# Performance work log

Hardware: AMD Instinct MI355X
Metric: run time of the kernel (lower is better)

## Reference

```python
import jax, jax.numpy as jnp
import numpy as np

EPS = 1e-3  # BN1d eps from norm_cfg


def _vfe_layer(x, W, gamma, beta, max_out, cat_max):
    """x: (N, M, Cin); W: (Cout, Cin) torch Linear layout; BN in training mode
    (batch stats over voxels N and points M per channel), then ReLU."""
    y = jnp.einsum('nmc,oc->nmo', x, W)            # (N, M, Cout)
    mean = y.mean(axis=(0, 1))                     # (Cout,)
    var = y.var(axis=(0, 1))                       # biased var, as BN uses
    y = (y - mean) * jax.lax.rsqrt(var + EPS) * gamma + beta
    pointwise = jax.nn.relu(y)                     # (N, M, Cout)
    if not max_out:
        return pointwise
    aggregated = pointwise.max(axis=1, keepdims=True)  # (N, 1, Cout)
    if not cat_max:
        return aggregated[:, 0, :]                 # (N, Cout)
    M = x.shape[1]
    repeated = jnp.broadcast_to(aggregated, (x.shape[0], M, aggregated.shape[2]))
    return jnp.concatenate([pointwise, repeated], axis=2)  # (N, M, 2*Cout)


def setup_inputs() -> dict:
    key = jax.random.key(0)
    ks = jax.random.split(key, 3)
    N, M, C = 20000, 64, 10
    return {
        'voxel_feats': jax.random.normal(ks[0], (N, M, C), dtype=jnp.float32),
        'W0': jax.random.normal(ks[1], (64, C), dtype=jnp.float32) * (1.0 / np.sqrt(C)),
        'gamma0': jnp.ones((64,), dtype=jnp.float32),
        'beta0': jnp.zeros((64,), dtype=jnp.float32),
        'W1': jax.random.normal(ks[2], (128, 128), dtype=jnp.float32) * (1.0 / np.sqrt(128)),
        'gamma1': jnp.ones((128,), dtype=jnp.float32),
        'beta1': jnp.zeros((128,), dtype=jnp.float32),
    }


def reference(voxel_feats, W0, gamma0, beta0, W1, gamma1, beta1):
    # layer 0: in=10 -> out=64, max_out=True, cat_max=True -> (N, M, 128)
    x = _vfe_layer(voxel_feats, W0, gamma0, beta0, max_out=True, cat_max=True)
    # layer 1 (last): in=128 -> out=128, max_out=True, cat_max=False -> (N, 128)
    x = _vfe_layer(x, W1, gamma1, beta1, max_out=True, cat_max=False)
    return x
```

## Files before the change

### kernel.cpp

```cpp
#include <hip/hip_runtime.h>

#define NVOX 20000
#define MPTS 64
#define CIN  10
#define NM   (NVOX*MPTS)
#define EPSBN 1e-3f

#define WS_SCALE0 0
#define WS_SHIFT0 64
#define WS_SCALE1 128
#define WS_SHIFT1 256

#define NB0   512
#define P0STR 72
#define NB1   1024
#define NBF   1536

typedef short bf16x8 __attribute__((ext_vector_type(8)));
typedef float f32x4  __attribute__((ext_vector_type(4)));

__device__ __forceinline__ unsigned short f2bf(float f) {
    union { float f; unsigned u; } v; v.f = f;
    unsigned r = v.u + 0x7FFFu + ((v.u >> 16) & 1u);
    return (unsigned short)(r >> 16);
}

__global__ __launch_bounds__(256) void k_stats0(const float* __restrict__ x,
                                                float* __restrict__ p0) {
    __shared__ float sm[4][P0STR];
    float sx[CIN];
    float sxx[55];
#pragma unroll
    for (int i = 0; i < CIN; i++) sx[i] = 0.f;
#pragma unroll
    for (int k = 0; k < 55; k++) sxx[k] = 0.f;

    const int t = threadIdx.x;
    const int tid = blockIdx.x * 256 + t;

    for (int g = tid; g < NM / 2; g += NB0 * 256) {
        const float4* xp = (const float4*)(x + (size_t)g * 20);
        float4 a = xp[0], b = xp[1], c = xp[2], d = xp[3], e = xp[4];
        float v0[CIN] = {a.x, a.y, a.z, a.w, b.x, b.y, b.z, b.w, c.x, c.y};
        float v1[CIN] = {c.z, c.w, d.x, d.y, d.z, d.w, e.x, e.y, e.z, e.w};
#pragma unroll
        for (int i = 0; i < CIN; i++) sx[i] += v0[i] + v1[i];
#pragma unroll
        for (int i = 0; i < CIN; i++)
#pragma unroll
            for (int j = 0; j <= i; j++)
                sxx[i * (i + 1) / 2 + j] += v0[i] * v0[j] + v1[i] * v1[j];
    }

    const int l = t & 63, w = t >> 6;
#pragma unroll
    for (int i = 0; i < CIN; i++) {
        float v = sx[i];
#pragma unroll
        for (int off = 32; off; off >>= 1) v += __shfl_xor(v, off, 64);
        if (l == 0) sm[w][i] = v;
    }
#pragma unroll
    for (int k = 0; k < 55; k++) {
        float v = sxx[k];
#pragma unroll
        for (int off = 32; off; off >>= 1) v += __shfl_xor(v, off, 64);
        if (l == 0) sm[w][10 + k] = v;
    }
    __syncthreads();
    if (t < 65)
        p0[blockIdx.x * P0STR + t] = sm[0][t] + sm[1][t] + sm[2][t] + sm[3][t];
}

__global__ void k_finalize0(const float* __restrict__ p0, float* __restrict__ ws,
                            const float* __restrict__ w0,
                            const float* __restrict__ gamma0, const float* __restrict__ beta0) {
    __shared__ float s[P0STR];
    const int t = threadIdx.x;
    if (t < 65) {
        float acc = 0.f;
#pragma unroll 8
        for (int r = 0; r < NB0; r++) acc += p0[r * P0STR + t];
        s[t] = acc;
    }
    __syncthreads();
    if (t < 64) {
        float w[CIN];
#pragma unroll
        for (int i = 0; i < CIN; i++) w[i] = w0[t * CIN + i];
        float m = 0.f;
#pragma unroll
        for (int i = 0; i < CIN; i++) m += w[i] * s[i];
        m *= (1.f / NM);
        float q = 0.f;
#pragma unroll
        for (int i = 0; i < CIN; i++)
#pragma unroll
            for (int j = 0; j <= i; j++)
                q += ((i == j) ? 1.f : 2.f) * w[i] * w[j] * s[10 + i * (i + 1) / 2 + j];
        q *= (1.f / NM);
        float var = q - m * m;
        float scale = gamma0[t] * rsqrtf(var + EPSBN);
        ws[WS_SCALE0 + t] = scale;
        ws[WS_SHIFT0 + t] = beta0[t] - m * scale;
    }
}

__global__ void k_finalize1(const float* __restrict__ p1, float* __restrict__ ws,
                            const float* __restrict__ gamma1, const float* __restrict__ beta1) {
    __shared__ float sm[2][4];
    const int c = blockIdx.x;
    const int t = threadIdx.x, l = t & 63, w = t >> 6;
    float s = 0.f, qq = 0.f;
#pragma unroll
    for (int r = t; r < NB1; r += 256) {
        s  += p1[(size_t)r * 256 + c];
        qq += p1[(size_t)r * 256 + 128 + c];
    }
#pragma unroll
    for (int off = 32; off; off >>= 1) { s += __shfl_xor(s, off, 64); qq += __shfl_xor(qq, off, 64); }
    if (l == 0) { sm[0][w] = s; sm[1][w] = qq; }
    __syncthreads();
    if (t == 0) {
        float S = sm[0][0] + sm[0][1] + sm[0][2] + sm[0][3];
        float Q = sm[1][0] + sm[1][1] + sm[1][2] + sm[1][3];
        float m = S * (1.f / NM);
        float var = Q * (1.f / NM) - m * m;
        float scale = gamma1[c] * rsqrtf(var + EPSBN);
        ws[WS_SCALE1 + c] = scale;
        ws[WS_SHIFT1 + c] = beta1[c] - m * scale;
    }
}

template <bool STATS>
__global__ __launch_bounds__(256) void k_pass(const float* __restrict__ x,
                                              const float* __restrict__ w0,
                                              const float* __restrict__ w1,
                                              const float* __restrict__ ws,
                                              float* __restrict__ pout) {
    __shared__ float xs[MPTS * CIN];
    __shared__ unsigned short zB[MPTS * 72];
    __shared__ unsigned short aggB[64];
    __shared__ float red[4 * 64];
    __shared__ float pbuf[256];

    const int t  = threadIdx.x;
    const int l  = t & 63;
    const int w  = t >> 6;
    const int lr = l & 15;
    const int lg = l >> 4;

    const int ch = t & 63;
    const int q  = t >> 6;
    float w0r[CIN];
#pragma unroll
    for (int i = 0; i < CIN; i++) w0r[i] = w0[ch * CIN + i];
    const float sc0 = ws[WS_SCALE0 + ch];
    const float sh0 = ws[WS_SHIFT0 + ch];

    bf16x8 wfrag[2][4];
#pragma unroll
    for (int njl = 0; njl < 2; njl++) {
        const float* wrow = w1 + (32 * w + 16 * njl + lr) * 128;
#pragma unroll
        for (int ks = 0; ks < 4; ks++) {
            float4 a = *(const float4*)(wrow + 32 * ks + 8 * lg);
            float4 b = *(const float4*)(wrow + 32 * ks + 8 * lg + 4);
            bf16x8 f;
            f[0] = (short)f2bf(a.x); f[1] = (short)f2bf(a.y);
            f[2] = (short)f2bf(a.z); f[3] = (short)f2bf(a.w);
            f[4] = (short)f2bf(b.x); f[5] = (short)f2bf(b.y);
            f[6] = (short)f2bf(b.z); f[7] = (short)f2bf(b.w);
            wfrag[njl][ks] = f;
        }
    }

    float sc1[2], sh1[2];
    if (!STATS) {
#pragma unroll
        for (int njl = 0; njl < 2; njl++) {
            int col = 32 * w + 16 * njl + lr;
            sc1[njl] = ws[WS_SCALE1 + col];
            sh1[njl] = ws[WS_SHIFT1 + col];
        }
    }
    float as_[2] = {0.f, 0.f}, aq[2] = {0.f, 0.f};

    const int nblk = STATS ? NB1 : NBF;
    for (int n = blockIdx.x; n < NVOX; n += nblk) {
        const float* xv = x + (size_t)n * (MPTS * CIN);
        if (t < 160) ((float4*)xs)[t] = ((const float4*)xv)[t];
        __syncthreads();

        float pm = 0.f;
#pragma unroll
        for (int k = 0; k < 16; k++) {
            int p = q * 16 + k;
            const float* xp = xs + p * CIN;
            float y = xp[0] * w0r[0] + xp[1] * w0r[1] + xp[2] * w0r[2] + xp[3] * w0r[3] +
                      xp[4] * w0r[4] + xp[5] * w0r[5] + xp[6] * w0r[6] + xp[7] * w0r[7] +
                      xp[8] * w0r[8] + xp[9] * w0r[9];
            float v = fmaxf(fmaf(y, sc0, sh0), 0.f);
            zB[p * 72 + ch] = f2bf(v);
            pm = fmaxf(pm, v);
        }
        red[q * 64 + ch] = pm;
        __syncthreads();
        if (t < 64) {
            float m = fmaxf(fmaxf(red[t], red[64 + t]), fmaxf(red[128 + t], red[192 + t]));
            aggB[t] = f2bf(m);
        }
        __syncthreads();

        bf16x8 afrag[4][2];
#pragma unroll
        for (int mi = 0; mi < 4; mi++)
#pragma unroll
            for (int ks = 0; ks < 2; ks++)
                afrag[mi][ks] = *(const bf16x8*)&zB[(16 * mi + lr) * 72 + 32 * ks + 8 * lg];
        bf16x8 gfrag[2];
#pragma unroll
        for (int ksh = 0; ksh < 2; ksh++)
            gfrag[ksh] = *(const bf16x8*)&aggB[32 * ksh + 8 * lg];

        f32x4 dacc[2];
#pragma unroll
        for (int njl = 0; njl < 2; njl++) {
            f32x4 zz = {0.f, 0.f, 0.f, 0.f};
            zz = __builtin_amdgcn_mfma_f32_16x16x32_bf16(gfrag[0], wfrag[njl][2], zz, 0, 0, 0);
            dacc[njl] = __builtin_amdgcn_mfma_f32_16x16x32_bf16(gfrag[1], wfrag[njl][3], zz, 0, 0, 0);
        }

        float vm[2] = {0.f, 0.f};
#pragma unroll
        for (int njl = 0; njl < 2; njl++) {
#pragma unroll
            for (int mi = 0; mi < 4; mi++) {
                f32x4 acc = dacc[njl];
                acc = __builtin_amdgcn_mfma_f32_16x16x32_bf16(afrag[mi][0], wfrag[njl][0], acc, 0, 0, 0);
                acc = __builtin_amdgcn_mfma_f32_16x16x32_bf16(afrag[mi][1], wfrag[njl][1], acc, 0, 0, 0);
                if (STATS) {
#pragma unroll
                    for (int r = 0; r < 4; r++) { as_[njl] += acc[r]; aq[njl] += acc[r] * acc[r]; }
                } else {
#pragma unroll
                    for (int r = 0; r < 4; r++)
                        vm[njl] = fmaxf(vm[njl], fmaxf(fmaf(acc[r], sc1[njl], sh1[njl]), 0.f));
                }
            }
        }

        if (!STATS) {
#pragma unroll
            for (int njl = 0; njl < 2; njl++) {
                float v = vm[njl];
                v = fmaxf(v, __shfl_xor(v, 16));
                v = fmaxf(v, __shfl_xor(v, 32));
                if (l < 16) pout[(size_t)n * 128 + 32 * w + 16 * njl + l] = v;
            }
        }
    }

    if (STATS) {
#pragma unroll
        for (int njl = 0; njl < 2; njl++) {
            float s = as_[njl];
            s += __shfl_xor(s, 16); s += __shfl_xor(s, 32);
            float qq = aq[njl];
            qq += __shfl_xor(qq, 16); qq += __shfl_xor(qq, 32);
            if (l < 16) {
                int col = 32 * w + 16 * njl + l;
                pbuf[col] = s;
                pbuf[128 + col] = qq;
            }
        }
        __syncthreads();
        pout[(size_t)blockIdx.x * 256 + t] = pbuf[t];
    }
}

extern "C" void kernel_launch(void* const* d_in, const int* in_sizes, int n_in,
                              void* d_out, int out_size, void* d_ws, size_t ws_size,
                              hipStream_t stream) {
    (void)in_sizes; (void)n_in; (void)out_size; (void)ws_size;
    const float* x      = (const float*)d_in[0];
    const float* W0     = (const float*)d_in[1];
    const float* gamma0 = (const float*)d_in[2];
    const float* beta0  = (const float*)d_in[3];
    const float* W1     = (const float*)d_in[4];
    const float* gamma1 = (const float*)d_in[5];
    const float* beta1  = (const float*)d_in[6];
    float* out = (float*)d_out;
    float* ws  = (float*)d_ws;

    k_stats0<<<NB0, 256, 0, stream>>>(x, out);
    k_finalize0<<<1, 256, 0, stream>>>(out, ws, W0, gamma0, beta0);
    k_pass<true><<<NB1, 256, 0, stream>>>(x, W0, W1, ws, out);
    k_finalize1<<<128, 256, 0, stream>>>(out, ws, gamma1, beta1);
    k_pass<false><<<NBF, 256, 0, stream>>>(x, W0, W1, ws, out);
}
```

Before: 244.0 us.

## Compute layer-0 linear+BN with MFMA and reduce voxel max in packed bf16

```diff
diff --git a/kernel.cpp b/kernel.cpp
--- a/kernel.cpp
+++ b/kernel.cpp
@@ -13,16 +13,27 @@
 
 #define NB0   512
 #define P0STR 72
-#define NB1   1024
-#define NBF   1536
+#define NB1   2000
+#define NBF   2000
 
 typedef short bf16x8 __attribute__((ext_vector_type(8)));
 typedef float f32x4  __attribute__((ext_vector_type(4)));
+typedef unsigned int u32x4 __attribute__((ext_vector_type(4)));
 
 __device__ __forceinline__ unsigned short f2bf(float f) {
     union { float f; unsigned u; } v; v.f = f;
     unsigned r = v.u + 0x7FFFu + ((v.u >> 16) & 1u);
     return (unsigned short)(r >> 16);
+}
+__device__ __forceinline__ unsigned cvtpk(float lo, float hi) {
+    unsigned d;
+    asm("v_cvt_pk_bf16_f32 %0, %1, %2" : "=v"(d) : "v"(lo), "v"(hi));
+    return d;
+}
+__device__ __forceinline__ unsigned pkmax(unsigned a, unsigned b) {
+    unsigned d;
+    asm("v_pk_max_u16 %0, %1, %2" : "=v"(d) : "v"(a), "v"(b));
+    return d;
 }
 
 __global__ __launch_bounds__(256) void k_stats0(const float* __restrict__ x,
@@ -112,7 +123,6 @@
     const int c = blockIdx.x;
     const int t = threadIdx.x, l = t & 63, w = t >> 6;
     float s = 0.f, qq = 0.f;
-#pragma unroll
     for (int r = t; r < NB1; r += 256) {
         s  += p1[(size_t)r * 256 + c];
         qq += p1[(size_t)r * 256 + 128 + c];
@@ -138,10 +148,9 @@
                                               const float* __restrict__ w1,
                                               const float* __restrict__ ws,
                                               float* __restrict__ pout) {
-    __shared__ float xs[MPTS * CIN];
+    __shared__ unsigned short xB[MPTS * 40];
     __shared__ unsigned short zB[MPTS * 72];
-    __shared__ unsigned short aggB[64];
-    __shared__ float red[4 * 64];
+    __shared__ unsigned short aggP[4 * 64];
     __shared__ float pbuf[256];
 
     const int t  = threadIdx.x;
@@ -150,13 +159,24 @@
     const int lr = l & 15;
     const int lg = l >> 4;
 
-    const int ch = t & 63;
-    const int q  = t >> 6;
-    float w0r[CIN];
-#pragma unroll
-    for (int i = 0; i < CIN; i++) w0r[i] = w0[ch * CIN + i];
-    const float sc0 = ws[WS_SCALE0 + ch];
-    const float sh0 = ws[WS_SHIFT0 + ch];
+    for (int i = t; i < MPTS * 40 / 2; i += 256) ((unsigned*)xB)[i] = 0u;
+    __syncthreads();
+    if (t < 64) xB[t * 40 + 10] = 0x3F80;
+
+    bf16x8 w0f[4];
+#pragma unroll
+    for (int mi = 0; mi < 4; mi++) {
+        int ch = 16 * mi + lr;
+        float sc = ws[WS_SCALE0 + ch], sh = ws[WS_SHIFT0 + ch];
+        bf16x8 f;
+#pragma unroll
+        for (int j = 0; j < 8; j++) {
+            int k = 8 * lg + j;
+            float v = (k < CIN) ? sc * w0[ch * CIN + k] : (k == CIN ? sh : 0.f);
+            f[j] = (short)f2bf(v);
+        }
+        w0f[mi] = f;
+    }
 
     bf16x8 wfrag[2][4];
 #pragma unroll
@@ -188,40 +208,79 @@
 
     const int nblk = STATS ? NB1 : NBF;
     for (int n = blockIdx.x; n < NVOX; n += nblk) {
-        const float* xv = x + (size_t)n * (MPTS * CIN);
-        if (t < 160) ((float4*)xs)[t] = ((const float4*)xv)[t];
+        if (t < 128) {
+            int p = t >> 1, h = t & 1;
+            const float* xp = x + (size_t)n * (MPTS * CIN) + p * CIN;
+            if (h == 0) {
+                float2 a = ((const float2*)xp)[0];
+                float2 b = ((const float2*)xp)[1];
+                uint2 d = { cvtpk(a.x, a.y), cvtpk(b.x, b.y) };
+                *(uint2*)&xB[p * 40] = d;
+            } else {
+                float2 a = ((const float2*)(xp + 4))[0];
+                float2 b = ((const float2*)(xp + 4))[1];
+                float2 c = ((const float2*)(xp + 4))[2];
+                uint2 d = { cvtpk(a.x, a.y), cvtpk(b.x, b.y) };
+                *(uint2*)&xB[p * 40 + 4] = d;
+                *(unsigned*)&xB[p * 40 + 8] = cvtpk(c.x, c.y);
+            }
+        }
         __syncthreads();
 
-        float pm = 0.f;
-#pragma unroll
-        for (int k = 0; k < 16; k++) {
-            int p = q * 16 + k;
-            const float* xp = xs + p * CIN;
-            float y = xp[0] * w0r[0] + xp[1] * w0r[1] + xp[2] * w0r[2] + xp[3] * w0r[3] +
-                      xp[4] * w0r[4] + xp[5] * w0r[5] + xp[6] * w0r[6] + xp[7] * w0r[7] +
-                      xp[8] * w0r[8] + xp[9] * w0r[9];
-            float v = fmaxf(fmaf(y, sc0, sh0), 0.f);
-            zB[p * 72 + ch] = f2bf(v);
-            pm = fmaxf(pm, v);
-        }
-        red[q * 64 + ch] = pm;
+        {
+            const int p = 16 * w + lr;
+            bf16x8 bx = *(const bf16x8*)&xB[p * 40 + 8 * lg];
+#pragma unroll
+            for (int mi = 0; mi < 4; mi++) {
+                f32x4 zz = {0.f, 0.f, 0.f, 0.f};
+                f32x4 a0 = __builtin_amdgcn_mfma_f32_16x16x32_bf16(w0f[mi], bx, zz, 0, 0, 0);
+                unsigned d0 = cvtpk(fmaxf(a0[0], 0.f), fmaxf(a0[1], 0.f));
+                unsigned d1 = cvtpk(fmaxf(a0[2], 0.f), fmaxf(a0[3], 0.f));
+                int chunk = 2 * mi + (lg >> 1);
+                int idx = p * 72 + ((chunk ^ (p & 7)) << 3) + ((lg & 1) << 2);
+                uint2 dd = {d0, d1};
+                *(uint2*)&zB[idx] = dd;
+            }
+        }
         __syncthreads();
-        if (t < 64) {
-            float m = fmaxf(fmaxf(red[t], red[64 + t]), fmaxf(red[128 + t], red[192 + t]));
-            aggB[t] = f2bf(m);
+
+        {
+            int cs = t & 7;
+            int pa = (t >> 3) * 2, pb = pa + 1;
+            u32x4 ra = *(const u32x4*)&zB[pa * 72 + ((cs ^ (pa & 7)) << 3)];
+            u32x4 rb = *(const u32x4*)&zB[pb * 72 + ((cs ^ (pb & 7)) << 3)];
+            u32x4 m;
+#pragma unroll
+            for (int k2 = 0; k2 < 4; k2++) m[k2] = pkmax(ra[k2], rb[k2]);
+#pragma unroll
+            for (int off = 8; off <= 32; off <<= 1)
+#pragma unroll
+                for (int k2 = 0; k2 < 4; k2++) m[k2] = pkmax(m[k2], __shfl_xor(m[k2], off));
+            if (l < 8) *(u32x4*)&aggP[w * 64 + l * 8] = m;
         }
         __syncthreads();
 
-        bf16x8 afrag[4][2];
-#pragma unroll
-        for (int mi = 0; mi < 4; mi++)
+        bf16x8 bz[4][2];
+#pragma unroll
+        for (int pj = 0; pj < 4; pj++) {
+            int p = 16 * pj + lr;
 #pragma unroll
             for (int ks = 0; ks < 2; ks++)
-                afrag[mi][ks] = *(const bf16x8*)&zB[(16 * mi + lr) * 72 + 32 * ks + 8 * lg];
+                bz[pj][ks] = *(const bf16x8*)&zB[p * 72 + (((4 * ks + lg) ^ (p & 7)) << 3)];
+        }
         bf16x8 gfrag[2];
 #pragma unroll
-        for (int ksh = 0; ksh < 2; ksh++)
-            gfrag[ksh] = *(const bf16x8*)&aggB[32 * ksh + 8 * lg];
+        for (int ks = 0; ks < 2; ks++) {
+            int sl = (4 * ks + lg) * 8;
+            u32x4 g = *(const u32x4*)&aggP[sl];
+#pragma unroll
+            for (int wv = 1; wv < 4; wv++) {
+                u32x4 h2 = *(const u32x4*)&aggP[wv * 64 + sl];
+#pragma unroll
+                for (int k2 = 0; k2 < 4; k2++) g[k2] = pkmax(g[k2], h2[k2]);
+            }
+            gfrag[ks] = __builtin_bit_cast(bf16x8, g);
+        }
 
         f32x4 dacc[2];
 #pragma unroll
@@ -237,8 +296,8 @@
 #pragma unroll
             for (int mi = 0; mi < 4; mi++) {
                 f32x4 acc = dacc[njl];
-                acc = __builtin_amdgcn_mfma_f32_16x16x32_bf16(afrag[mi][0], wfrag[njl][0], acc, 0, 0, 0);
-                acc = __builtin_amdgcn_mfma_f32_16x16x32_bf16(afrag[mi][1], wfrag[njl][1], acc, 0, 0, 0);
+                acc = __builtin_amdgcn_mfma_f32_16x16x32_bf16(bz[mi][0], wfrag[njl][0], acc, 0, 0, 0);
+                acc = __builtin_amdgcn_mfma_f32_16x16x32_bf16(bz[mi][1], wfrag[njl][1], acc, 0, 0, 0);
                 if (STATS) {
 #pragma unroll
                     for (int r = 0; r < 4; r++) { as_[njl] += acc[r]; aq[njl] += acc[r] * acc[r]; }
```

Result: no change. 242.8 us (-0.5%).
